# Kernel tuning notes

Measured on AMD Instinct MI355X. Metric: run time of the kernel, lower is better.

## Reference

```python
import jax, jax.numpy as jnp
import numpy as np

D_CONV = 4
D_STATE = 16
DT_RANK = 64


def _silu(x):
    return x * jax.nn.sigmoid(x)


def setup_inputs() -> dict:
    key = jax.random.key(0)
    ks = jax.random.split(key, 10)
    B, L, dim = 2, 1024, 1024
    d_inner = 2 * dim
    s = lambda fan: 1.0 / np.sqrt(fan)
    inp = {
        "x": jax.random.normal(ks[0], (B, L, dim), jnp.float32),
        "ln_w": jnp.ones((dim,), jnp.float32),
        "ln_b": jnp.zeros((dim,), jnp.float32),
        "w_in": jax.random.normal(ks[1], (2 * d_inner, dim), jnp.float32) * s(dim),
        "conv_w": jax.random.normal(ks[2], (d_inner, D_CONV), jnp.float32) * s(D_CONV),
        "conv_b": jnp.zeros((d_inner,), jnp.float32),
        "w_xproj": jax.random.normal(ks[3], (DT_RANK + 2 * D_STATE, d_inner), jnp.float32) * s(d_inner),
        "w_dt": jax.random.normal(ks[4], (d_inner, DT_RANK), jnp.float32) * s(DT_RANK),
        "b_dt": jax.random.normal(ks[5], (d_inner,), jnp.float32) * 0.1,
        # S4D-real init: A = -(1..d_state) per channel
        "a_log": jnp.tile(jnp.log(jnp.arange(1, D_STATE + 1, dtype=jnp.float32)), (d_inner, 1)),
        "d_skip": jnp.ones((d_inner,), jnp.float32),
        "w_out": jax.random.normal(ks[6], (dim, d_inner), jnp.float32) * s(d_inner),
    }
    return inp


def reference(x, ln_w, ln_b, w_in, conv_w, conv_b, w_xproj, w_dt, b_dt, a_log, d_skip, w_out):
    B, L, dim = x.shape
    residual = x

    # LayerNorm
    mu = jnp.mean(x, axis=-1, keepdims=True)
    var = jnp.mean((x - mu) ** 2, axis=-1, keepdims=True)
    xn = (x - mu) * jax.lax.rsqrt(var + 1e-5) * ln_w + ln_b

    # in_proj -> (x_ssm, z) each (B, L, d_inner)
    xz = jnp.einsum("bld,ed->ble", xn, w_in)
    d_inner = xz.shape[-1] // 2
    xs, z = xz[..., :d_inner], xz[..., d_inner:]

    # depthwise causal conv1d (kernel D_CONV) + SiLU
    xp = jnp.pad(xs, ((0, 0), (D_CONV - 1, 0), (0, 0)))
    xc = conv_b
    for k in range(D_CONV):
        xc = xc + conv_w[:, k] * xp[:, k : k + L, :]
    u = _silu(xc)  # (B, L, d_inner)

    # x_proj -> dt, B, C
    x_dbl = jnp.einsum("ble,re->blr", u, w_xproj)
    dt_r = x_dbl[..., :DT_RANK]
    B_ssm = x_dbl[..., DT_RANK : DT_RANK + D_STATE]         # (B, L, n)
    C_ssm = x_dbl[..., DT_RANK + D_STATE :]                 # (B, L, n)

    dt = jax.nn.softplus(jnp.einsum("blr,er->ble", dt_r, w_dt) + b_dt)  # (B, L, d_inner)

    A = -jnp.exp(a_log)  # (d_inner, n)
    deltaA = jnp.exp(jnp.einsum("ble,en->blen", dt, A))            # (B, L, e, n)
    deltaBu = jnp.einsum("ble,bln,ble->blen", dt, B_ssm, u)        # (B, L, e, n)

    # selective scan over L
    def step(h, ins):
        dA_t, dBu_t, C_t = ins
        h = dA_t * h + dBu_t                       # (B, e, n)
        y = jnp.einsum("ben,bn->be", h, C_t)
        return h, y

    h0 = jnp.zeros((B, d_inner, D_STATE), xs.dtype)
    _, ys = jax.lax.scan(
        step,
        h0,
        (deltaA.transpose(1, 0, 2, 3), deltaBu.transpose(1, 0, 2, 3), C_ssm.transpose(1, 0, 2)),
    )
    y = ys.transpose(1, 0, 2) + u * d_skip         # (B, L, e)

    y = y * _silu(z)
    out = jnp.einsum("ble,de->bld", y, w_out)
    return residual + out
```

## Files before the change

### kernel.cpp

```cpp
#include <hip/hip_runtime.h>
#include <hip/hip_bf16.h>


#define LC 32
#define NCHUNK 32

typedef short bf16x8 __attribute__((ext_vector_type(8)));
typedef float f32x4  __attribute__((ext_vector_type(4)));

static __device__ __forceinline__ float siluf(float x) { return x / (1.f + __expf(-x)); }
static __device__ __forceinline__ unsigned short f2bf(float f) {
    unsigned int u = __float_as_uint(f);
    unsigned int r = (u + 0x7fffu + ((u >> 16) & 1u)) >> 16;
    return (unsigned short)r;
}
static __device__ __forceinline__ void gload_lds16(const void* g, void* l) {
    __builtin_amdgcn_global_load_lds(
        (const __attribute__((address_space(1))) void*)g,
        (__attribute__((address_space(3))) void*)l, 16, 0, 0);
}

__global__ __launch_bounds__(256) void f2b_all(
    const float* __restrict__ w_in,  unsigned short* __restrict__ w_in_b,
    const float* __restrict__ w_out, unsigned short* __restrict__ w_out_b,
    const float* __restrict__ w_dt,  unsigned short* __restrict__ w_dt_b)
{
    int i = blockIdx.x * 256 + threadIdx.x;
    const float* in; unsigned short* outp; int j;
    if (i < 1048576)      { in = w_in;  outp = w_in_b;  j = i; }
    else if (i < 1572864) { in = w_out; outp = w_out_b; j = i - 1048576; }
    else if (i < 1605632) { in = w_dt;  outp = w_dt_b;  j = i - 1572864; }
    else return;
    float4 v = reinterpret_cast<const float4*>(in)[j];
    ushort4 o = { f2bf(v.x), f2bf(v.y), f2bf(v.z), f2bf(v.w) };
    reinterpret_cast<ushort4*>(outp)[j] = o;
}

__global__ __launch_bounds__(256) void ln_kernel(
    const float* __restrict__ x,
    const float* __restrict__ w,
    const float* __restrict__ bias,
    unsigned short* __restrict__ xn)
{
    int m = blockIdx.x, tid = threadIdx.x;
    const float4* xr = reinterpret_cast<const float4*>(x) + (size_t)m * 256;
    float4 r = xr[tid];
    float f0 = r.x, f1 = r.y, f2 = r.z, f3 = r.w;
    float s  = f0 + f1 + f2 + f3;
    float s2 = f0*f0 + f1*f1 + f2*f2 + f3*f3;
    #pragma unroll
    for (int off = 32; off > 0; off >>= 1) {
        s  += __shfl_down(s, off);
        s2 += __shfl_down(s2, off);
    }
    __shared__ float red[8];
    if ((tid & 63) == 0) { red[tid >> 6] = s; red[4 + (tid >> 6)] = s2; }
    __syncthreads();
    float st = red[0] + red[1] + red[2] + red[3];
    float qt = red[4] + red[5] + red[6] + red[7];
    float mu   = st * (1.f / 1024.f);
    float var  = qt * (1.f / 1024.f) - mu * mu;
    float rstd = rsqrtf(var + 1e-5f);
    float4 wv = reinterpret_cast<const float4*>(w)[tid];
    float4 bv = reinterpret_cast<const float4*>(bias)[tid];
    ushort4 o = { f2bf((f0 - mu) * rstd * wv.x + bv.x),
                  f2bf((f1 - mu) * rstd * wv.y + bv.y),
                  f2bf((f2 - mu) * rstd * wv.z + bv.z),
                  f2bf((f3 - mu) * rstd * wv.w + bv.w) };
    reinterpret_cast<ushort4*>(xn + (size_t)m * 1024)[tid] = o;
}

__global__ __launch_bounds__(256) void gemm_bf16_nt(
    const unsigned short* __restrict__ A, int lda,
    const unsigned short* __restrict__ B, int ldb,
    int Kslice,
    float* __restrict__ C, int ldc,
    const float* __restrict__ bias,
    const float* __restrict__ resid,
    int ep, size_t Cstride)
{
    __shared__ short As[2 * 128 * 32];
    __shared__ short Bs[2 * 64 * 32];
    int tid = threadIdx.x;
    int z = blockIdx.z;
    A += (size_t)z * Kslice;
    B += (size_t)z * Kslice;
    C += (size_t)z * Cstride;
    int m0 = blockIdx.y * 128, n0 = blockIdx.x * 64;
    int lane = tid & 63, wave = tid >> 6;
    int wm = (wave >> 1) * 64, wn = (wave & 1) * 32;
    int frow = lane & 15, fq = lane >> 4;

    f32x4 acc[4][2] = {};

    int lrow = lane >> 2;
    int scol = (lane & 3) * 8;
    const unsigned short* AgL = A + (size_t)(m0 + wave * 32 + lrow) * lda + scol;
    const unsigned short* BgL = B + (size_t)(n0 + wave * 16 + lrow) * ldb + scol;
    int aoff = (wave * 32) * 32;
    int boff = (wave * 16) * 32;

    gload_lds16(AgL,                      As + aoff);
    gload_lds16(AgL + (size_t)16 * lda,   As + aoff + 16 * 32);
    gload_lds16(BgL,                      Bs + boff);

    int cur = 0;
    for (int k0 = 0; k0 < Kslice; k0 += 32) {
        __syncthreads();
        int nk = k0 + 32;
        if (nk < Kslice) {
            int nxt = cur ^ 1;
            gload_lds16(AgL + nk,                     As + nxt * 4096 + aoff);
            gload_lds16(AgL + (size_t)16 * lda + nk,  As + nxt * 4096 + aoff + 16 * 32);
            gload_lds16(BgL + nk,                     Bs + nxt * 2048 + boff);
        }
        const short* Ac = As + cur * 4096;
        const short* Bc = Bs + cur * 2048;
        bf16x8 af[4], bfr[2];
        #pragma unroll
        for (int i = 0; i < 4; ++i)
            af[i] = *reinterpret_cast<const bf16x8*>(Ac + (wm + i * 16 + frow) * 32 + fq * 8);
        #pragma unroll
        for (int j = 0; j < 2; ++j)
            bfr[j] = *reinterpret_cast<const bf16x8*>(Bc + (wn + j * 16 + frow) * 32 + fq * 8);
        #pragma unroll
        for (int i = 0; i < 4; ++i)
            #pragma unroll
            for (int j = 0; j < 2; ++j)
                acc[i][j] = __builtin_amdgcn_mfma_f32_16x16x32_bf16(af[i], bfr[j], acc[i][j], 0, 0, 0);
        cur ^= 1;
    }

    int cn = lane & 15, rq = (lane >> 4) * 4;
    #pragma unroll
    for (int i = 0; i < 4; ++i) {
        #pragma unroll
        for (int j = 0; j < 2; ++j) {
            #pragma unroll
            for (int r = 0; r < 4; ++r) {
                int row = m0 + wm + i * 16 + rq + r;
                int col = n0 + wn + j * 16 + cn;
                float v = acc[i][j][r];
                if (ep == 0) {
                    C[(size_t)row * ldc + col] = v;
                } else if (ep == 1) {
                    v += bias[col];
                    v = (v > 20.f) ? v : log1pf(__expf(v));
                    C[(size_t)row * ldc + col] = v;
                } else {
                    v += resid[(size_t)row * ldc + col];
                    C[(size_t)row * ldc + col] = v;
                }
            }
        }
    }
}

__global__ __launch_bounds__(256) void out_reduce(
    const float* __restrict__ part, const float* __restrict__ x,
    float* __restrict__ out)
{
    int i = blockIdx.x * 256 + threadIdx.x;
    float4 s = reinterpret_cast<const float4*>(x)[i];
    #pragma unroll
    for (int z = 0; z < 4; ++z) {
        float4 p = reinterpret_cast<const float4*>(part + (size_t)z * 2097152)[i];
        s.x += p.x; s.y += p.y; s.z += p.z; s.w += p.w;
    }
    reinterpret_cast<float4*>(out)[i] = s;
}

__global__ __launch_bounds__(256) void xproj_splitk(
    const float* __restrict__ A,
    const float* __restrict__ B,
    float* __restrict__ part)
{
    __shared__ float As[16][68];
    __shared__ float Bs[16][100];
    int tid = threadIdx.x;
    int m0 = blockIdx.x * 64;
    int k0 = blockIdx.y * 128;
    int tx = tid & 15;
    int ty = tid >> 4;
    float acc[4][6] = {};
    int arow = tid >> 2, akg = (tid & 3) << 2;
    int brow1 = (256 + tid) >> 2, bkg1 = ((256 + tid) & 3) << 2;

    for (int ks = 0; ks < 128; ks += 16) {
        float4 av = *reinterpret_cast<const float4*>(A + (size_t)(m0 + arow) * 2048 + k0 + ks + akg);
        float4 bv0 = make_float4(0.f, 0.f, 0.f, 0.f), bv1 = bv0;
        if (arow < 96)  bv0 = *reinterpret_cast<const float4*>(B + (size_t)arow * 2048 + k0 + ks + akg);
        if (brow1 < 96) bv1 = *reinterpret_cast<const float4*>(B + (size_t)brow1 * 2048 + k0 + ks + bkg1);
        __syncthreads();
        As[akg + 0][arow] = av.x; As[akg + 1][arow] = av.y;
        As[akg + 2][arow] = av.z; As[akg + 3][arow] = av.w;
        if (arow < 96) {
            Bs[akg + 0][arow] = bv0.x; Bs[akg + 1][arow] = bv0.y;
            Bs[akg + 2][arow] = bv0.z; Bs[akg + 3][arow] = bv0.w;
        }
        if (brow1 < 96) {
            Bs[bkg1 + 0][brow1] = bv1.x; Bs[bkg1 + 1][brow1] = bv1.y;
            Bs[bkg1 + 2][brow1] = bv1.z; Bs[bkg1 + 3][brow1] = bv1.w;
        }
        __syncthreads();
        #pragma unroll
        for (int k = 0; k < 16; ++k) {
            float aa[4], bb[6];
            #pragma unroll
            for (int i = 0; i < 4; ++i) aa[i] = As[k][ty * 4 + i];
            #pragma unroll
            for (int j = 0; j < 6; ++j) bb[j] = Bs[k][tx * 6 + j];
            #pragma unroll
            for (int i = 0; i < 4; ++i)
                #pragma unroll
                for (int j = 0; j < 6; ++j)
                    acc[i][j] = fmaf(aa[i], bb[j], acc[i][j]);
        }
    }
    float* p = part + (size_t)blockIdx.y * 196608;
    #pragma unroll
    for (int i = 0; i < 4; ++i)
        #pragma unroll
        for (int j = 0; j < 6; ++j)
            p[(size_t)(m0 + ty * 4 + i) * 96 + tx * 6 + j] = acc[i][j];
}

__global__ __launch_bounds__(256) void xproj_reduce(
    const float* __restrict__ part, float* __restrict__ xdbl,
    unsigned short* __restrict__ dtr)
{
    int i = blockIdx.x * 256 + threadIdx.x;
    float s = 0.f;
    #pragma unroll
    for (int sd = 0; sd < 16; ++sd) s += part[(size_t)sd * 196608 + i];
    xdbl[i] = s;
    int m = i / 96, col = i - m * 96;
    if (col < 64) dtr[(size_t)m * 64 + col] = f2bf(s);
}

__global__ __launch_bounds__(256) void conv_silu_kernel(
    const float* __restrict__ xz,
    const float* __restrict__ cw,
    const float* __restrict__ cb,
    float* __restrict__ u)
{
    int idx = blockIdx.x * 256 + threadIdx.x;
    int e = idx & 2047;
    int m = idx >> 11;
    int l = m & 1023;
    float acc = cb[e];
    #pragma unroll
    for (int k = 0; k < 4; ++k) {
        int ls = l - 3 + k;
        if (ls >= 0)
            acc += cw[e * 4 + k] * xz[(size_t)(m - 3 + k) * 4096 + e];
    }
    u[(size_t)m * 2048 + e] = siluf(acc);
}

__global__ __launch_bounds__(256) void scan_part1(
    const float* __restrict__ dt,
    const float* __restrict__ u,
    const float* __restrict__ xdbl,
    const float* __restrict__ a_log,
    float* __restrict__ hpart,
    float* __restrict__ Aprod)
{
    int tid = threadIdx.x;
    int ch = tid >> 2, ng = tid & 3;
    int bid = blockIdx.x;
    int c = bid & 31, et = (bid >> 5) & 31, b = bid >> 10;
    int e = et * 64 + ch;
    float4 al = *reinterpret_cast<const float4*>(a_log + e * 16 + ng * 4);
    float A0 = -__expf(al.x), A1 = -__expf(al.y), A2 = -__expf(al.z), A3 = -__expf(al.w);
    size_t rbase = (size_t)b * 1024 + c * LC;
    const float* dt_p = dt + rbase * 2048 + e;
    const float* u_p  = u  + rbase * 2048 + e;
    const float* b_p  = xdbl + rbase * 96 + 64 + ng * 4;
    float h0 = 0.f, h1 = 0.f, h2 = 0.f, h3 = 0.f;
    float P0 = 1.f, P1 = 1.f, P2 = 1.f, P3 = 1.f;
    float dt_c = dt_p[0];
    float u_c  = u_p[0];
    float4 B_c = *reinterpret_cast<const float4*>(b_p);
    #pragma unroll 4
    for (int l = 0; l < LC; ++l) {
        float dt_n = dt_p[(size_t)(l + 1) * 2048];
        float u_n  = u_p[(size_t)(l + 1) * 2048];
        float4 B_n = *reinterpret_cast<const float4*>(b_p + (size_t)(l + 1) * 96);
        float du = dt_c * u_c;
        float d0 = __expf(dt_c * A0), d1 = __expf(dt_c * A1);
        float d2 = __expf(dt_c * A2), d3 = __expf(dt_c * A3);
        h0 = fmaf(d0, h0, du * B_c.x); P0 *= d0;
        h1 = fmaf(d1, h1, du * B_c.y); P1 *= d1;
        h2 = fmaf(d2, h2, du * B_c.z); P2 *= d2;
        h3 = fmaf(d3, h3, du * B_c.w); P3 *= d3;
        dt_c = dt_n; u_c = u_n; B_c = B_n;
    }
    size_t oidx = (size_t)c * 65536 + ((size_t)b * 2048 + e) * 16 + ng * 4;
    *reinterpret_cast<float4*>(hpart + oidx) = make_float4(h0, h1, h2, h3);
    *reinterpret_cast<float4*>(Aprod + oidx) = make_float4(P0, P1, P2, P3);
}

__global__ __launch_bounds__(256) void scan_combine(
    const float* __restrict__ hpart,
    const float* __restrict__ Aprod,
    float* __restrict__ hinit)
{
    int t = (blockIdx.x * 256 + threadIdx.x) * 4;
    float4 h = make_float4(0.f, 0.f, 0.f, 0.f);
    #pragma unroll
    for (int c = 0; c < NCHUNK; ++c) {
        *reinterpret_cast<float4*>(hinit + (size_t)c * 65536 + t) = h;
        float4 P = *reinterpret_cast<const float4*>(Aprod + (size_t)c * 65536 + t);
        float4 hp = *reinterpret_cast<const float4*>(hpart + (size_t)c * 65536 + t);
        h.x = fmaf(P.x, h.x, hp.x);
        h.y = fmaf(P.y, h.y, hp.y);
        h.z = fmaf(P.z, h.z, hp.z);
        h.w = fmaf(P.w, h.w, hp.w);
    }
}

__global__ __launch_bounds__(256) void scan_part2(
    const float* __restrict__ dt,
    const float* __restrict__ u,
    const float* __restrict__ xdbl,
    const float* __restrict__ xz,
    const float* __restrict__ a_log,
    const float* __restrict__ d_skip,
    const float* __restrict__ hinit,
    unsigned short* __restrict__ y)
{
    int tid = threadIdx.x;
    int ch = tid >> 2, ng = tid & 3;
    int bid = blockIdx.x;
    int c = bid & 31, et = (bid >> 5) & 31, b = bid >> 10;
    int e = et * 64 + ch;
    float4 al = *reinterpret_cast<const float4*>(a_log + e * 16 + ng * 4);
    float A0 = -__expf(al.x), A1 = -__expf(al.y), A2 = -__expf(al.z), A3 = -__expf(al.w);
    float dsk = d_skip[e];
    size_t rbase = (size_t)b * 1024 + c * LC;
    const float* dt_p = dt + rbase * 2048 + e;
    const float* u_p  = u  + rbase * 2048 + e;
    const float* z_p  = xz + rbase * 4096 + 2048 + e;
    const float* bc_p = xdbl + rbase * 96 + 64 + ng * 4;
    unsigned short* y_p = y + rbase * 2048 + e;
    size_t oidx = (size_t)c * 65536 + ((size_t)b * 2048 + e) * 16 + ng * 4;
    float4 hi = *reinterpret_cast<const float4*>(hinit + oidx);
    float h0 = hi.x, h1 = hi.y, h2 = hi.z, h3 = hi.w;
    float dt_c = dt_p[0];
    float u_c  = u_p[0];
    float4 B_c = *reinterpret_cast<const float4*>(bc_p);
    float4 C_c = *reinterpret_cast<const float4*>(bc_p + 16);
    #pragma unroll 4
    for (int l = 0; l < LC; ++l) {
        float dt_n = dt_p[(size_t)(l + 1) * 2048];
        float u_n  = u_p[(size_t)(l + 1) * 2048];
        float4 B_n = *reinterpret_cast<const float4*>(bc_p + (size_t)(l + 1) * 96);
        float4 C_n = *reinterpret_cast<const float4*>(bc_p + (size_t)(l + 1) * 96 + 16);
        float du = dt_c * u_c;
        float d0 = __expf(dt_c * A0), d1 = __expf(dt_c * A1);
        float d2 = __expf(dt_c * A2), d3 = __expf(dt_c * A3);
        h0 = fmaf(d0, h0, du * B_c.x);
        h1 = fmaf(d1, h1, du * B_c.y);
        h2 = fmaf(d2, h2, du * B_c.z);
        h3 = fmaf(d3, h3, du * B_c.w);
        float p = h0 * C_c.x + h1 * C_c.y + h2 * C_c.z + h3 * C_c.w;
        p += __shfl_xor(p, 1);
        p += __shfl_xor(p, 2);
        if (ng == 0) {
            float zv = z_p[(size_t)l * 4096];
            y_p[(size_t)l * 2048] = f2bf((p + u_c * dsk) * siluf(zv));
        }
        dt_c = dt_n; u_c = u_n; B_c = B_n; C_c = C_n;
    }
}

extern "C" void kernel_launch(void* const* d_in, const int* in_sizes, int n_in,
                              void* d_out, int out_size, void* d_ws, size_t ws_size,
                              hipStream_t stream) {
    const float* x       = (const float*)d_in[0];
    const float* ln_w    = (const float*)d_in[1];
    const float* ln_b    = (const float*)d_in[2];
    const float* w_in    = (const float*)d_in[3];
    const float* conv_w  = (const float*)d_in[4];
    const float* conv_b  = (const float*)d_in[5];
    const float* w_xproj = (const float*)d_in[6];
    const float* w_dt    = (const float*)d_in[7];
    const float* b_dt    = (const float*)d_in[8];
    const float* a_log   = (const float*)d_in[9];
    const float* d_skip  = (const float*)d_in[10];
    const float* w_out   = (const float*)d_in[11];
    float* out = (float*)d_out;

    float* ws = (float*)d_ws;
    unsigned short* xn_b    = (unsigned short*)(ws);
    float* xz    = ws + 1048576;
    float* u     = ws + 9437184;
    float* xdbl  = ws + 13631488;
    float* dt    = ws + 13828096;
    float* hpart = ws + 18022400;
    float* Aprod = ws + 20119552;
    float* hinit = ws + 22216704;
    float* xpart = ws + 18022400;
    float* opart = xz;
    unsigned short* y_b     = (unsigned short*)(ws + 18022400);
    unsigned short* w_in_b  = (unsigned short*)(ws + 21168128);
    unsigned short* w_dt_b  = (unsigned short*)(ws + 24313856);
    unsigned short* dtr_b   = (unsigned short*)(ws + 24379392);
    unsigned short* w_out_b = (unsigned short*)(ws + 24444928);

    f2b_all<<<6272, 256, 0, stream>>>(w_in, w_in_b, w_out, w_out_b, w_dt, w_dt_b);
    ln_kernel<<<2048, 256, 0, stream>>>(x, ln_w, ln_b, xn_b);
    gemm_bf16_nt<<<dim3(64, 16, 1), 256, 0, stream>>>(xn_b, 1024, w_in_b, 1024, 1024,
                                                      xz, 4096, nullptr, nullptr, 0, 0);
    conv_silu_kernel<<<16384, 256, 0, stream>>>(xz, conv_w, conv_b, u);
    xproj_splitk<<<dim3(32, 16), 256, 0, stream>>>(u, w_xproj, xpart);
    xproj_reduce<<<768, 256, 0, stream>>>(xpart, xdbl, dtr_b);
    gemm_bf16_nt<<<dim3(32, 16, 1), 256, 0, stream>>>(dtr_b, 64, w_dt_b, 64, 64,
                                                      dt, 2048, b_dt, nullptr, 1, 0);
    scan_part1<<<2048, 256, 0, stream>>>(dt, u, xdbl, a_log, hpart, Aprod);
    scan_combine<<<64, 256, 0, stream>>>(hpart, Aprod, hinit);
    scan_part2<<<2048, 256, 0, stream>>>(dt, u, xdbl, xz, a_log, d_skip, hinit, y_b);
    gemm_bf16_nt<<<dim3(16, 16, 4), 256, 0, stream>>>(y_b, 2048, w_out_b, 2048, 512,
                                                      opart, 1024, nullptr, nullptr, 0, 2097152);
    out_reduce<<<2048, 256, 0, stream>>>(opart, x, out);
}
```

Before: 279.6 us.

## Store intermediate activations xz, u, dt in bf16 instead of fp32

```diff
diff --git a/kernel.cpp b/kernel.cpp
--- a/kernel.cpp
+++ b/kernel.cpp
@@ -13,6 +13,9 @@
     unsigned int u = __float_as_uint(f);
     unsigned int r = (u + 0x7fffu + ((u >> 16) & 1u)) >> 16;
     return (unsigned short)r;
+}
+static __device__ __forceinline__ float bfb(unsigned short u) {
+    return __uint_as_float(((unsigned int)u) << 16);
 }
 static __device__ __forceinline__ void gload_lds16(const void* g, void* l) {
     __builtin_amdgcn_global_load_lds(
@@ -74,9 +77,8 @@
     const unsigned short* __restrict__ A, int lda,
     const unsigned short* __restrict__ B, int ldb,
     int Kslice,
-    float* __restrict__ C, int ldc,
+    float* __restrict__ C, unsigned short* __restrict__ Cb, int ldc,
     const float* __restrict__ bias,
-    const float* __restrict__ resid,
     int ep, size_t Cstride)
 {
     __shared__ short As[2 * 128 * 32];
@@ -146,10 +148,9 @@
                 } else if (ep == 1) {
                     v += bias[col];
                     v = (v > 20.f) ? v : log1pf(__expf(v));
-                    C[(size_t)row * ldc + col] = v;
+                    Cb[(size_t)row * ldc + col] = f2bf(v);
                 } else {
-                    v += resid[(size_t)row * ldc + col];
-                    C[(size_t)row * ldc + col] = v;
+                    Cb[(size_t)row * ldc + col] = f2bf(v);
                 }
             }
         }
@@ -171,7 +172,7 @@
 }
 
 __global__ __launch_bounds__(256) void xproj_splitk(
-    const float* __restrict__ A,
+    const unsigned short* __restrict__ A,
     const float* __restrict__ B,
     float* __restrict__ part)
 {
@@ -187,7 +188,8 @@
     int brow1 = (256 + tid) >> 2, bkg1 = ((256 + tid) & 3) << 2;
 
     for (int ks = 0; ks < 128; ks += 16) {
-        float4 av = *reinterpret_cast<const float4*>(A + (size_t)(m0 + arow) * 2048 + k0 + ks + akg);
+        ushort4 au = *reinterpret_cast<const ushort4*>(A + (size_t)(m0 + arow) * 2048 + k0 + ks + akg);
+        float4 av = make_float4(bfb(au.x), bfb(au.y), bfb(au.z), bfb(au.w));
         float4 bv0 = make_float4(0.f, 0.f, 0.f, 0.f), bv1 = bv0;
         if (arow < 96)  bv0 = *reinterpret_cast<const float4*>(B + (size_t)arow * 2048 + k0 + ks + akg);
         if (brow1 < 96) bv1 = *reinterpret_cast<const float4*>(B + (size_t)brow1 * 2048 + k0 + ks + bkg1);
@@ -239,10 +241,10 @@
 }
 
 __global__ __launch_bounds__(256) void conv_silu_kernel(
-    const float* __restrict__ xz,
+    const unsigned short* __restrict__ xz,
     const float* __restrict__ cw,
     const float* __restrict__ cb,
-    float* __restrict__ u)
+    unsigned short* __restrict__ u)
 {
     int idx = blockIdx.x * 256 + threadIdx.x;
     int e = idx & 2047;
@@ -253,14 +255,14 @@
     for (int k = 0; k < 4; ++k) {
         int ls = l - 3 + k;
         if (ls >= 0)
-            acc += cw[e * 4 + k] * xz[(size_t)(m - 3 + k) * 4096 + e];
-    }
-    u[(size_t)m * 2048 + e] = siluf(acc);
+            acc += cw[e * 4 + k] * bfb(xz[(size_t)(m - 3 + k) * 4096 + e]);
+    }
+    u[(size_t)m * 2048 + e] = f2bf(siluf(acc));
 }
 
 __global__ __launch_bounds__(256) void scan_part1(
-    const float* __restrict__ dt,
-    const float* __restrict__ u,
+    const unsigned short* __restrict__ dt,
+    const unsigned short* __restrict__ u,
     const float* __restrict__ xdbl,
     const float* __restrict__ a_log,
     float* __restrict__ hpart,
@@ -274,18 +276,18 @@
     float4 al = *reinterpret_cast<const float4*>(a_log + e * 16 + ng * 4);
     float A0 = -__expf(al.x), A1 = -__expf(al.y), A2 = -__expf(al.z), A3 = -__expf(al.w);
     size_t rbase = (size_t)b * 1024 + c * LC;
-    const float* dt_p = dt + rbase * 2048 + e;
-    const float* u_p  = u  + rbase * 2048 + e;
+    const unsigned short* dt_p = dt + rbase * 2048 + e;
+    const unsigned short* u_p  = u  + rbase * 2048 + e;
     const float* b_p  = xdbl + rbase * 96 + 64 + ng * 4;
     float h0 = 0.f, h1 = 0.f, h2 = 0.f, h3 = 0.f;
     float P0 = 1.f, P1 = 1.f, P2 = 1.f, P3 = 1.f;
-    float dt_c = dt_p[0];
-    float u_c  = u_p[0];
+    float dt_c = bfb(dt_p[0]);
+    float u_c  = bfb(u_p[0]);
     float4 B_c = *reinterpret_cast<const float4*>(b_p);
     #pragma unroll 4
     for (int l = 0; l < LC; ++l) {
-        float dt_n = dt_p[(size_t)(l + 1) * 2048];
-        float u_n  = u_p[(size_t)(l + 1) * 2048];
+        float dt_n = bfb(dt_p[(size_t)(l + 1) * 2048]);
+        float u_n  = bfb(u_p[(size_t)(l + 1) * 2048]);
         float4 B_n = *reinterpret_cast<const float4*>(b_p + (size_t)(l + 1) * 96);
         float du = dt_c * u_c;
         float d0 = __expf(dt_c * A0), d1 = __expf(dt_c * A1);
@@ -321,10 +323,10 @@
 }
 
 __global__ __launch_bounds__(256) void scan_part2(
-    const float* __restrict__ dt,
-    const float* __restrict__ u,
+    const unsigned short* __restrict__ dt,
+    const unsigned short* __restrict__ u,
     const float* __restrict__ xdbl,
-    const float* __restrict__ xz,
+    const unsigned short* __restrict__ xz,
     const float* __restrict__ a_log,
     const float* __restrict__ d_skip,
     const float* __restrict__ hinit,
@@ -339,22 +341,22 @@
     float A0 = -__expf(al.x), A1 = -__expf(al.y), A2 = -__expf(al.z), A3 = -__expf(al.w);
     float dsk = d_skip[e];
     size_t rbase = (size_t)b * 1024 + c * LC;
-    const float* dt_p = dt + rbase * 2048 + e;
-    const float* u_p  = u  + rbase * 2048 + e;
-    const float* z_p  = xz + rbase * 4096 + 2048 + e;
+    const unsigned short* dt_p = dt + rbase * 2048 + e;
+    const unsigned short* u_p  = u  + rbase * 2048 + e;
+    const unsigned short* z_p  = xz + rbase * 4096 + 2048 + e;
     const float* bc_p = xdbl + rbase * 96 + 64 + ng * 4;
     unsigned short* y_p = y + rbase * 2048 + e;
     size_t oidx = (size_t)c * 65536 + ((size_t)b * 2048 + e) * 16 + ng * 4;
     float4 hi = *reinterpret_cast<const float4*>(hinit + oidx);
     float h0 = hi.x, h1 = hi.y, h2 = hi.z, h3 = hi.w;
-    float dt_c = dt_p[0];
-    float u_c  = u_p[0];
+    float dt_c = bfb(dt_p[0]);
+    float u_c  = bfb(u_p[0]);
     float4 B_c = *reinterpret_cast<const float4*>(bc_p);
     float4 C_c = *reinterpret_cast<const float4*>(bc_p + 16);
     #pragma unroll 4
     for (int l = 0; l < LC; ++l) {
-        float dt_n = dt_p[(size_t)(l + 1) * 2048];
-        float u_n  = u_p[(size_t)(l + 1) * 2048];
+        float dt_n = bfb(dt_p[(size_t)(l + 1) * 2048]);
+        float u_n  = bfb(u_p[(size_t)(l + 1) * 2048]);
         float4 B_n = *reinterpret_cast<const float4*>(bc_p + (size_t)(l + 1) * 96);
         float4 C_n = *reinterpret_cast<const float4*>(bc_p + (size_t)(l + 1) * 96 + 16);
         float du = dt_c * u_c;
@@ -368,7 +370,7 @@
         p += __shfl_xor(p, 1);
         p += __shfl_xor(p, 2);
         if (ng == 0) {
-            float zv = z_p[(size_t)l * 4096];
+            float zv = bfb(z_p[(size_t)l * 4096]);
             y_p[(size_t)l * 2048] = f2bf((p + u_c * dsk) * siluf(zv));
         }
         dt_c = dt_n; u_c = u_n; B_c = B_n; C_c = C_n;
@@ -394,34 +396,34 @@
 
     float* ws = (float*)d_ws;
     unsigned short* xn_b    = (unsigned short*)(ws);
-    float* xz    = ws + 1048576;
-    float* u     = ws + 9437184;
-    float* xdbl  = ws + 13631488;
-    float* dt    = ws + 13828096;
-    float* hpart = ws + 18022400;
-    float* Aprod = ws + 20119552;
-    float* hinit = ws + 22216704;
-    float* xpart = ws + 18022400;
-    float* opart = xz;
-    unsigned short* y_b     = (unsigned short*)(ws + 18022400);
-    unsigned short* w_in_b  = (unsigned short*)(ws + 21168128);
-    unsigned short* w_dt_b  = (unsigned short*)(ws + 24313856);
-    unsigned short* dtr_b   = (unsigned short*)(ws + 24379392);
-    unsigned short* w_out_b = (unsigned short*)(ws + 24444928);
+    unsigned short* xz_b    = (unsigned short*)(ws + 1048576);
+    unsigned short* u_b     = (unsigned short*)(ws + 5242880);
+    float* xdbl  = ws + 7340032;
+    unsigned short* dt_b    = (unsigned short*)(ws + 7536640);
+    float* hpart = ws + 9633792;
+    float* Aprod = ws + 11730944;
+    float* hinit = ws + 13828096;
+    unsigned short* y_b     = (unsigned short*)(ws + 15925248);
+    unsigned short* w_in_b  = (unsigned short*)(ws + 18022400);
+    unsigned short* w_out_b = (unsigned short*)(ws + 20119552);
+    unsigned short* w_dt_b  = (unsigned short*)(ws + 21168128);
+    unsigned short* dtr_b   = (unsigned short*)(ws + 21233664);
+    float* xpart = ws + 9633792;
+    float* opart = ws + 1048576;
 
     f2b_all<<<6272, 256, 0, stream>>>(w_in, w_in_b, w_out, w_out_b, w_dt, w_dt_b);
     ln_kernel<<<2048, 256, 0, stream>>>(x, ln_w, ln_b, xn_b);
     gemm_bf16_nt<<<dim3(64, 16, 1), 256, 0, stream>>>(xn_b, 1024, w_in_b, 1024, 1024,
-                                                      xz, 4096, nullptr, nullptr, 0, 0);
-    conv_silu_kernel<<<16384, 256, 0, stream>>>(xz, conv_w, conv_b, u);
-    xproj_splitk<<<dim3(32, 16), 256, 0, stream>>>(u, w_xproj, xpart);
+                                                      nullptr, xz_b, 4096, nullptr, 3, 0);
+    conv_silu_kernel<<<16384, 256, 0, stream>>>(xz_b, conv_w, conv_b, u_b);
+    xproj_splitk<<<dim3(32, 16), 256, 0, stream>>>(u_b, w_xproj, xpart);
     xproj_reduce<<<768, 256, 0, stream>>>(xpart, xdbl, dtr_b);
     gemm_bf16_nt<<<dim3(32, 16, 1), 256, 0, stream>>>(dtr_b, 64, w_dt_b, 64, 64,
-                                                      dt, 2048, b_dt, nullptr, 1, 0);
-    scan_part1<<<2048, 256, 0, stream>>>(dt, u, xdbl, a_log, hpart, Aprod);
+                                                      nullptr, dt_b, 2048, b_dt, 1, 0);
+    scan_part1<<<2048, 256, 0, stream>>>(dt_b, u_b, xdbl, a_log, hpart, Aprod);
     scan_combine<<<64, 256, 0, stream>>>(hpart, Aprod, hinit);
-    scan_part2<<<2048, 256, 0, stream>>>(dt, u, xdbl, xz, a_log, d_skip, hinit, y_b);
+    scan_part2<<<2048, 256, 0, stream>>>(dt_b, u_b, xdbl, xz_b, a_log, d_skip, hinit, y_b);
     gemm_bf16_nt<<<dim3(16, 16, 4), 256, 0, stream>>>(y_b, 2048, w_out_b, 2048, 512,
-                                                      opart, 1024, nullptr, nullptr, 0, 2097152);
+                                                      opart, nullptr, 1024, nullptr, 0, 2097152);
     out_reduce<<<2048, 256, 0, stream>>>(opart, x, out);
 }
```

Result: no change. 280.2 us (+0.2%).
